# Kernel tuning notes

Measured on AMD Instinct MI355X. Metric: run time of the kernel, lower is better.

Reference implementation:

```python
import jax, jax.numpy as jnp
import numpy as np

C = 64          # in_channel
K = 3           # kernel_size
STRIDE = 1
PAD = 1


def make_weight():
    # torch.diag(ones(k*k)).repeat(C,1).reshape(C*k*k, 1, K, K)
    kk = K * K
    return jnp.tile(jnp.eye(kk, dtype=jnp.float32), (C, 1)).reshape(C * kk, 1, K, K)


def setup_inputs() -> dict:
    key = jax.random.key(0)
    x = jax.random.normal(key, (16, C, 112, 112), dtype=jnp.float32)
    return {"x": x, "weight": make_weight()}


def reference(x, weight):
    # Depthwise (grouped) conv with fixed diagonal-identity kernel == patch unfold.
    # Output: [N, C*K*K, H_out, W_out]
    return jax.lax.conv_general_dilated(
        x, weight,
        window_strides=(STRIDE, STRIDE),
        padding=[(PAD, PAD), (PAD, PAD)],
        dimension_numbers=("NCHW", "OIHW", "NCHW"),
        feature_group_count=C,
    )
```

## Files before the change

kernel.cpp:

```cpp
#include <hip/hip_runtime.h>


#define NN 16
#define CC 64
#define HH 112
#define WW 112
#define W4C 28
#define PLANE  (HH * WW)
#define PLANE4 (HH * W4C)
#define NPLANES (NN * CC * 9)

typedef float v4f __attribute__((ext_vector_type(4)));

__global__ __launch_bounds__(256) void unfold9_planes(const float* __restrict__ x,
                                                      float* __restrict__ out) {
    unsigned bid = blockIdx.x;
    unsigned p = (bid & 7u) * (NPLANES / 8u) + (bid >> 3);

    unsigned cj = p % (CC * 9);
    unsigned n  = p / (CC * 9);
    unsigned c  = cj / 9u;
    unsigned j  = cj % 9u;
    int dh = (int)(j / 3u) - 1;
    int dw = (int)(j % 3u) - 1;

    const float* __restrict__ xp = x + ((size_t)n * CC + c) * PLANE;
    float* __restrict__ op = out + (size_t)p * PLANE;

    for (unsigned pos = threadIdx.x; pos < PLANE4; pos += 256u) {
        unsigned h  = pos / W4C;
        unsigned w4 = pos % W4C;
        int sh = (int)h + dh;
        v4f v;
        if (sh < 0 || sh >= HH) {
            v = (v4f){0.f, 0.f, 0.f, 0.f};
        } else {
            const float* __restrict__ row = xp + (unsigned)sh * WW;
            unsigned wb = w4 * 4u;
            v4f m = *reinterpret_cast<const v4f*>(row + wb);
            if (dw == 0) {
                v = m;
            } else if (dw < 0) {
                float l = (w4 > 0u) ? row[wb - 1u] : 0.f;
                v = (v4f){l, m.x, m.y, m.z};
            } else {
                float r = (w4 < W4C - 1u) ? row[wb + 4u] : 0.f;
                v = (v4f){m.y, m.z, m.w, r};
            }
        }
        *reinterpret_cast<v4f*>(op + (size_t)pos * 4u) = v;
    }
}

extern "C" void kernel_launch(void* const* d_in, const int* in_sizes, int n_in,
                              void* d_out, int out_size, void* d_ws, size_t ws_size,
                              hipStream_t stream) {
    const float* x = (const float*)d_in[0];
    float* out = (float*)d_out;
    unfold9_planes<<<NPLANES, 256, 0, stream>>>(x, out);
}
```

Measured before the change: 526.0 us.

## Stage input row tiles in LDS and emit all nine shifted planes per block

Each block now loads a 28-row tile of one input channel, with halo rows and zero padding, into shared memory once. It then writes all nine shifted output planes from that tile, replacing the old one-block-per-output-plane scheme that re-read the input from global memory nine times. This trades redundant global and L2 reads for LDS traffic and a barrier. Grid size drops to 4 blocks per channel, each with more work, and the old interleaved block-to-plane mapping is gone.

```diff
diff --git a/kernel.cpp b/kernel.cpp
--- a/kernel.cpp
+++ b/kernel.cpp
@@ -8,47 +8,59 @@
 #define W4C 28
 #define PLANE  (HH * WW)
 #define PLANE4 (HH * W4C)
-#define NPLANES (NN * CC * 9)
+#define RPB 28
+#define LROWS (RPB + 2)
+#define LDS_F4 (LROWS * W4C)
+#define TPB 256
 
 typedef float v4f __attribute__((ext_vector_type(4)));
 
-__global__ __launch_bounds__(256) void unfold9_planes(const float* __restrict__ x,
-                                                      float* __restrict__ out) {
+__global__ __launch_bounds__(TPB) void unfold9_lds(const float* __restrict__ x,
+                                                   float* __restrict__ out) {
+    __shared__ float lds[LROWS * WW];
+
     unsigned bid = blockIdx.x;
-    unsigned p = (bid & 7u) * (NPLANES / 8u) + (bid >> 3);
+    unsigned q   = bid & 3u;
+    unsigned pb  = bid >> 2;
+    unsigned h0  = q * RPB;
 
-    unsigned cj = p % (CC * 9);
-    unsigned n  = p / (CC * 9);
-    unsigned c  = cj / 9u;
-    unsigned j  = cj % 9u;
-    int dh = (int)(j / 3u) - 1;
-    int dw = (int)(j % 3u) - 1;
+    const v4f* __restrict__ xp4 = reinterpret_cast<const v4f*>(x) + (size_t)pb * PLANE4;
+    v4f* lds4 = reinterpret_cast<v4f*>(lds);
 
-    const float* __restrict__ xp = x + ((size_t)n * CC + c) * PLANE;
-    float* __restrict__ op = out + (size_t)p * PLANE;
+    int gstart = (int)h0 * W4C - W4C;
+    for (unsigned t = threadIdx.x; t < LDS_F4; t += TPB) {
+        int g = gstart + (int)t;
+        v4f v = (v4f){0.f, 0.f, 0.f, 0.f};
+        if (g >= 0 && g < PLANE4) v = xp4[g];
+        lds4[t] = v;
+    }
+    __syncthreads();
 
-    for (unsigned pos = threadIdx.x; pos < PLANE4; pos += 256u) {
-        unsigned h  = pos / W4C;
-        unsigned w4 = pos % W4C;
-        int sh = (int)h + dh;
-        v4f v;
-        if (sh < 0 || sh >= HH) {
-            v = (v4f){0.f, 0.f, 0.f, 0.f};
-        } else {
-            const float* __restrict__ row = xp + (unsigned)sh * WW;
-            unsigned wb = w4 * 4u;
-            v4f m = *reinterpret_cast<const v4f*>(row + wb);
+    size_t obase = (size_t)pb * 9u * PLANE + (size_t)h0 * WW;
+#pragma unroll
+    for (int j = 0; j < 9; ++j) {
+        const int dh = j / 3 - 1;
+        const int dw = j % 3 - 1;
+        float* __restrict__ op = out + obase + (size_t)j * PLANE;
+        for (unsigned pos = threadIdx.x; pos < RPB * W4C; pos += TPB) {
+            unsigned qr = pos / W4C;
+            unsigned w4 = pos % W4C;
+            unsigned r  = qr + 1u + (unsigned)(dh + 0);
+            r = (unsigned)((int)qr + 1 + dh);
+            const float* row = lds + r * WW;
+            v4f m = *reinterpret_cast<const v4f*>(row + w4 * 4u);
+            v4f v;
             if (dw == 0) {
                 v = m;
             } else if (dw < 0) {
-                float l = (w4 > 0u) ? row[wb - 1u] : 0.f;
+                float l = (w4 > 0u) ? row[w4 * 4u - 1u] : 0.f;
                 v = (v4f){l, m.x, m.y, m.z};
             } else {
-                float r = (w4 < W4C - 1u) ? row[wb + 4u] : 0.f;
-                v = (v4f){m.y, m.z, m.w, r};
+                float rr = (w4 < W4C - 1u) ? row[w4 * 4u + 4u] : 0.f;
+                v = (v4f){m.y, m.z, m.w, rr};
             }
+            *reinterpret_cast<v4f*>(op + (size_t)pos * 4u) = v;
         }
-        *reinterpret_cast<v4f*>(op + (size_t)pos * 4u) = v;
     }
 }
 
@@ -57,5 +69,7 @@
                               hipStream_t stream) {
     const float* x = (const float*)d_in[0];
     float* out = (float*)d_out;
-    unfold9_planes<<<NPLANES, 256, 0, stream>>>(x, out);
+
+    const unsigned blocks = NN * CC * 4u;
+    unfold9_lds<<<blocks, TPB, 0, stream>>>(x, out);
 }
```

Result: faster. 492.4 us (-6.4%).
